# Performance work log

Hardware: AMD Instinct MI355X
Metric: run time of the kernel (lower is better)

## Reference

```python
import jax, jax.numpy as jnp
import numpy as np

# Jamba mamba mixer dims
H = 4096      # hidden_size
D = 8192      # intermediate_size = mamba_expand * hidden_size
N = 16        # ssm_state_size (mamba_d_state)
K = 4         # conv_kernel_size (mamba_d_conv)
R = 256       # time_step_rank (mamba_dt_rank)
BATCH = 1
L = 2048
EPS = 1e-6


def setup_inputs() -> dict:
    key = jax.random.key(0)
    ks = jax.random.split(key, 10)
    s = 0.02
    return {
        "hidden_states": jax.random.normal(ks[0], (BATCH, L, H), jnp.float32),
        "W_in": jax.random.normal(ks[1], (2 * D, H), jnp.float32) * s,
        "conv_w": jax.random.normal(ks[2], (D, K), jnp.float32) * s,
        "conv_b": jax.random.normal(ks[3], (D,), jnp.float32) * s,
        "Wx": jax.random.normal(ks[4], (R + 2 * N, D), jnp.float32) * s,
        "dt_ln_w": jnp.ones((R,), jnp.float32),
        "b_ln_w": jnp.ones((N,), jnp.float32),
        "c_ln_w": jnp.ones((N,), jnp.float32),
        "Wdt": jax.random.normal(ks[5], (D, R), jnp.float32) * s,
        "dt_bias": jax.random.normal(ks[6], (D,), jnp.float32) * s,
        "A": -jnp.exp(jax.random.normal(ks[7], (D, N), jnp.float32) * 0.5),  # A = -exp(A_log)
        "D_param": jnp.ones((D,), jnp.float32),
        "W_out": jax.random.normal(ks[8], (H, D), jnp.float32) * s,
    }


def _rmsnorm(x, w):
    return x * jax.lax.rsqrt(jnp.mean(x * x, axis=-1, keepdims=True) + EPS) * w


def reference(hidden_states, W_in, conv_w, conv_b, Wx, dt_ln_w, b_ln_w, c_ln_w,
              Wdt, dt_bias, A, D_param, W_out):
    # in_proj -> [B, L, 2D]; split into ssm branch and gate
    proj = hidden_states @ W_in.T
    u, gate = jnp.split(proj, 2, axis=-1)

    # causal depthwise conv1d over sequence dim, then SiLU (causal_conv1d_fn)
    x = jnp.transpose(u, (0, 2, 1))  # [B, D, L]
    x = jax.lax.conv_general_dilated(
        x, conv_w[:, None, :], window_strides=(1,), padding=[(K - 1, 0)],
        dimension_numbers=("NCH", "OIH", "NCH"), feature_group_count=D)
    u = jax.nn.silu(jnp.transpose(x, (0, 2, 1)) + conv_b)  # [B, L, D]

    # x_proj -> dt / B / C with RMSNorms
    ssm_p = u @ Wx.T  # [B, L, R + 2N]
    dt, Bm, Cm = jnp.split(ssm_p, [R, R + N], axis=-1)
    dt = _rmsnorm(dt, dt_ln_w)
    Bm = _rmsnorm(Bm, b_ln_w)
    Cm = _rmsnorm(Cm, c_ln_w)

    # dt_proj (skip_bias_add: bias folded into softplus, delta_softplus=True)
    delta = jax.nn.softplus(dt @ Wdt.T + dt_bias)  # [B, L, D]

    # selective scan: state [B, D, N], recurrence over L
    def step(state, xs):
        d_t, B_t, C_t, u_t = xs  # [B,D], [B,N], [B,N], [B,D]
        dA = jnp.exp(d_t[..., None] * A)                       # [B, D, N]
        state = dA * state + (d_t * u_t)[..., None] * B_t[:, None, :]
        y_t = jnp.einsum("bdn,bn->bd", state, C_t)
        return state, y_t

    init = jnp.zeros((hidden_states.shape[0], D, N), hidden_states.dtype)
    xs = (jnp.swapaxes(delta, 0, 1), jnp.swapaxes(Bm, 0, 1),
          jnp.swapaxes(Cm, 0, 1), jnp.swapaxes(u, 0, 1))
    _, ys = jax.lax.scan(step, init, xs)  # ys: [L, B, D]

    y = jnp.swapaxes(ys, 0, 1) + u * D_param   # skip connection u * D
    y = y * jax.nn.silu(gate)                  # gated output
    return y @ W_out.T                         # out_proj -> [B, L, H]
```

## Files before the change

kernel.cpp:

```cpp
#include <hip/hip_runtime.h>
#include <stdint.h>


#define LSEQ 2048
#define HDIM 4096
#define DDIM 8192
#define NST  16
#define NPAD 384
#define NC   32
#define CLEN 64
#define XZK  16

typedef __bf16 bf16x8 __attribute__((ext_vector_type(8)));
typedef float  f32x4  __attribute__((ext_vector_type(4)));

__device__ __forceinline__ ushort f2b(float f) {
  uint32_t x = __float_as_uint(f);
  x += 0x7FFFu + ((x >> 16) & 1u);
  return (ushort)(x >> 16);
}
__device__ __forceinline__ float b2f(ushort u) {
  return __uint_as_float(((uint32_t)u) << 16);
}
__device__ __forceinline__ float b2f_lo(uint u) {
  return __uint_as_float(u << 16);
}
__device__ __forceinline__ float b2f_hi(uint u) {
  return __uint_as_float(u & 0xFFFF0000u);
}

__device__ __forceinline__ void gload_lds16(const ushort* g, ushort* l) {
  __builtin_amdgcn_global_load_lds(
      (const __attribute__((address_space(1))) void*)g,
      (__attribute__((address_space(3))) void*)l, 16, 0, 0);
}

__global__ __launch_bounds__(256) void cvt_kernel(const float* __restrict__ s,
                                                  ushort* __restrict__ d,
                                                  size_t n8) {
  size_t i = (size_t)blockIdx.x * 256 + threadIdx.x;
  if (i >= n8) return;
  const float4* sp = (const float4*)s;
  float4 a = sp[2 * i], b = sp[2 * i + 1];
  union { ushort us[8]; uint4 v; } u;
  u.us[0] = f2b(a.x); u.us[1] = f2b(a.y); u.us[2] = f2b(a.z); u.us[3] = f2b(a.w);
  u.us[4] = f2b(b.x); u.us[5] = f2b(b.y); u.us[6] = f2b(b.z); u.us[7] = f2b(b.w);
  ((uint4*)d)[i] = u.v;
}

template <int MODE, int OUT>
__global__ __launch_bounds__(512, 2) void gemm8p(
    const ushort* __restrict__ A, const ushort* __restrict__ Bw,
    void* __restrict__ Cv, int M, int N, int ldk, int Kc,
    size_t bOffZ, size_t cOffZ) {
  __shared__ __align__(16) ushort As[2][256 * 64];
  __shared__ __align__(16) ushort Bs[2][256 * 64];
  const int tid  = threadIdx.x;
  const int lane = tid & 63;
  const int w    = tid >> 6;
  const int wr   = w >> 2;
  const int wc   = w & 3;

  int mt, nt, zz;
  size_t boff = 0, coff = 0;
  if (MODE == 0) {
    const int bid2 = blockIdx.y * gridDim.x + blockIdx.x;
    const int k8 = bid2 & 7, j = bid2 >> 3;
    mt = j & 7;
    nt = k8 * (gridDim.x >> 3) + (j >> 3);
    zz = 0;
    boff = (size_t)blockIdx.z * bOffZ;
    coff = (size_t)blockIdx.z * cOffZ;
  } else {
    const int glob = (blockIdx.z * gridDim.y + blockIdx.y) * gridDim.x + blockIdx.x;
    const int k8 = glob & 7, j = glob >> 3;
    mt = j & 7;
    nt = (k8 >> 1) * 4 + (j >> 3);
    zz = k8 & 1;
  }
  const int m0 = mt * 256, n0 = nt * 256;
  const int kbeg = zz * Kc;
  const int NT = Kc >> 6;

  const int srck = (lane & 7) ^ ((lane >> 3) & 7);
  const int astripe = w >> 2, awl = w & 3;
  const int arow_st = astripe * 128 + awl * 8 + (lane >> 3);
  const ushort* Abase = A + (size_t)(m0 + arow_st) * ldk + kbeg + srck * 8;
  const int aldsb = (astripe * 128 + awl * 8) * 64;
  const int brow_st = w * 8 + (lane >> 3);
  const ushort* Bbase = Bw + boff + (size_t)(n0 + brow_st) * ldk + kbeg + srck * 8;
  const int bldsb = (w * 8) * 64;

  const int lrow = lane & 15;
  const int kch  = lane >> 4;
  const int axor = lrow & 7;

  auto stA = [&](int buf, int kt, int q) {
    gload_lds16(Abase + (size_t)q * 32 * ldk + kt * 64,
                &As[buf][aldsb + q * 32 * 64]);
  };
  auto stB = [&](int buf, int kt, int half, int jj) {
    gload_lds16(Bbase + (size_t)(half * 128 + jj * 64) * ldk + kt * 64,
                &Bs[buf][bldsb + (half * 128 + jj * 64) * 64]);
  };
  auto rdA = [&](int buf, int mi, int sl) -> bf16x8 {
    int arow = wr * 128 + mi * 16 + lrow;
    int s4 = sl * 4 + kch;
    return *(const bf16x8*)&As[buf][arow * 64 + ((s4 ^ axor) << 3)];
  };
  auto rdB = [&](int buf, int ni, int sl) -> bf16x8 {
    int brow = wc * 64 + ni * 16 + lrow;
    int s4 = sl * 4 + kch;
    return *(const bf16x8*)&Bs[buf][brow * 64 + ((s4 ^ axor) << 3)];
  };

  f32x4 acc[8][4] = {};
  bf16x8 afr[2][2][2];
  bf16x8 bfr[2][4][2];

#define RDAQ(BUF, Q, AP)                                                      \
  { _Pragma("unroll") for (int m2 = 0; m2 < 2; ++m2)                          \
      _Pragma("unroll") for (int sl = 0; sl < 2; ++sl)                        \
        afr[AP][m2][sl] = rdA(BUF, (Q) * 2 + m2, sl); }
#define RDBALL(BUF, BP)                                                       \
  { _Pragma("unroll") for (int ni = 0; ni < 4; ++ni)                          \
      _Pragma("unroll") for (int sl = 0; sl < 2; ++sl)                        \
        bfr[BP][ni][sl] = rdB(BUF, ni, sl); }
#define MFMA16(MQ, AP, BP)                                                    \
  { asm volatile("s_barrier" ::: "memory");                                   \
    __builtin_amdgcn_s_setprio(1);                                            \
    _Pragma("unroll") for (int sl = 0; sl < 2; ++sl)                          \
      _Pragma("unroll") for (int m2 = 0; m2 < 2; ++m2)                        \
        _Pragma("unroll") for (int ni = 0; ni < 4; ++ni)                      \
          acc[(MQ) * 2 + m2][ni] = __builtin_amdgcn_mfma_f32_16x16x32_bf16(   \
              afr[AP][m2][sl], bfr[BP][ni][sl], acc[(MQ) * 2 + m2][ni],       \
              0, 0, 0);                                                       \
    __builtin_amdgcn_s_setprio(0); }

  stB(0, 0, 0, 0); stB(0, 0, 0, 1); stB(0, 0, 1, 0); stB(0, 0, 1, 1);
  stA(0, 0, 0); stA(0, 0, 1); stA(0, 0, 2); stA(0, 0, 3);
  stB(1, 1, 0, 0); stB(1, 1, 0, 1); stB(1, 1, 1, 0); stB(1, 1, 1, 1);
  stA(1, 1, 0); stA(1, 1, 1); stA(1, 1, 2); stA(1, 1, 3);
  asm volatile("s_waitcnt vmcnt(8)" ::: "memory");
  asm volatile("s_barrier" ::: "memory");
  RDBALL(0, 0);
  RDAQ(0, 0, 1);

  for (int t = 0; t < NT; t += 2) {
    const int t2 = (t + 2 < NT) ? t + 2 : 0;
    const int t3 = (t + 3 < NT) ? t + 3 : 0;
    RDAQ(0, 1, 0);
    stB(0, t2, 0, 0); stB(0, t2, 0, 1);
    MFMA16(0, 1, 0);
    RDAQ(0, 2, 1);
    stB(0, t2, 1, 0); stB(0, t2, 1, 1);
    MFMA16(1, 0, 0);
    RDAQ(0, 3, 0);
    stA(0, t2, 0); stA(0, t2, 1);
    MFMA16(2, 1, 0);
    asm volatile("s_waitcnt vmcnt(6)" ::: "memory");
    RDBALL(1, 1);
    RDAQ(1, 0, 1);
    stA(0, t2, 2); stA(0, t2, 3);
    MFMA16(3, 0, 0);
    RDAQ(1, 1, 0);
    stB(1, t3, 0, 0); stB(1, t3, 0, 1);
    MFMA16(0, 1, 1);
    RDAQ(1, 2, 1);
    stB(1, t3, 1, 0); stB(1, t3, 1, 1);
    MFMA16(1, 0, 1);
    RDAQ(1, 3, 0);
    stA(1, t3, 0); stA(1, t3, 1);
    MFMA16(2, 1, 1);
    asm volatile("s_waitcnt vmcnt(6)" ::: "memory");
    RDBALL(0, 0);
    RDAQ(0, 0, 1);
    stA(1, t3, 2); stA(1, t3, 3);
    MFMA16(3, 0, 1);
  }
#undef RDAQ
#undef RDBALL
#undef MFMA16

  asm volatile("s_waitcnt vmcnt(0)" ::: "memory");
  float*  C  = (float*) Cv + (size_t)zz * M * N + coff;
  ushort* Cb = (ushort*)Cv + (size_t)zz * M * N + coff;
#pragma unroll
  for (int mi = 0; mi < 8; ++mi) {
    int row0 = m0 + wr * 128 + mi * 16 + kch * 4;
#pragma unroll
    for (int ni = 0; ni < 4; ++ni) {
      int col = n0 + wc * 64 + ni * 16 + lrow;
#pragma unroll
      for (int q_ = 0; q_ < 4; ++q_) {
        if (OUT == 0)
          C[(size_t)(row0 + q_) * N + col] = acc[mi][ni][q_];
        else
          Cb[(size_t)(row0 + q_) * N + col] = f2b(acc[mi][ni][q_]);
      }
    }
  }
}

template <int EPI, int OBF>
__global__ __launch_bounds__(256) void gemm_nt(
    const ushort* __restrict__ A, const ushort* __restrict__ Bw,
    void* __restrict__ Cv, int M, int N, int ldk, int Kc,
    const float* __restrict__ bias) {
  __shared__ __align__(16) ushort As[128 * 64];
  __shared__ __align__(16) ushort Bs[128 * 64];
  const int tid  = threadIdx.x;
  const int lane = tid & 63;
  const int wid  = tid >> 6;
  const int wr = wid >> 1, wc = wid & 1;
  const int m0 = blockIdx.y * 128, n0 = blockIdx.x * 128;
  const int kbeg = blockIdx.z * Kc;
  float*  C  = (float*) Cv + (size_t)blockIdx.z * M * N;
  ushort* Cb = (ushort*)Cv + (size_t)blockIdx.z * M * N;
  const int rr0 = tid >> 3;
  const int sl  = tid & 7;
  const int lrow = lane & 15;
  const int lks  = lane >> 4;

  f32x4 acc[4][4] = {};

  for (int k0 = kbeg; k0 < kbeg + Kc; k0 += 64) {
#pragma unroll
    for (int i = 0; i < 4; ++i) {
      int rr  = i * 32 + rr0;
      int ksl = sl ^ (rr & 7);
      const ushort* ga = A  + (size_t)(m0 + rr) * ldk + k0 + ksl * 8;
      const ushort* gb = Bw + (size_t)(n0 + rr) * ldk + k0 + ksl * 8;
      ushort* la = As + (i * 256 + (wid << 6)) * 8;
      ushort* lb = Bs + (i * 256 + (wid << 6)) * 8;
      gload_lds16(ga, la);
      gload_lds16(gb, lb);
    }
    __syncthreads();
#pragma unroll
    for (int kc = 0; kc < 2; ++kc) {
      bf16x8 av[4], bv[4];
#pragma unroll
      for (int mi = 0; mi < 4; ++mi) {
        int row = wr * 64 + mi * 16 + lrow;
        int ks  = kc * 4 + lks;
        av[mi] = *(const bf16x8*)(As + row * 64 + ((ks ^ (row & 7)) << 3));
      }
#pragma unroll
      for (int ni = 0; ni < 4; ++ni) {
        int row = wc * 64 + ni * 16 + lrow;
        int ks  = kc * 4 + lks;
        bv[ni] = *(const bf16x8*)(Bs + row * 64 + ((ks ^ (row & 7)) << 3));
      }
#pragma unroll
      for (int mi = 0; mi < 4; ++mi)
#pragma unroll
        for (int ni = 0; ni < 4; ++ni)
          acc[mi][ni] = __builtin_amdgcn_mfma_f32_16x16x32_bf16(
              av[mi], bv[ni], acc[mi][ni], 0, 0, 0);
    }
    __syncthreads();
  }

#pragma unroll
  for (int mi = 0; mi < 4; ++mi) {
    int row0 = m0 + wr * 64 + mi * 16 + (lks << 2);
#pragma unroll
    for (int ni = 0; ni < 4; ++ni) {
      int col = n0 + wc * 64 + ni * 16 + lrow;
      float bcol = 0.f;
      if (EPI == 1) bcol = bias[col];
#pragma unroll
      for (int q = 0; q < 4; ++q) {
        float v = acc[mi][ni][q];
        if (EPI == 1) {
          v += bcol;
          v = (v > 20.f) ? v : log1pf(__expf(v));
        }
        if (OBF == 0) C [(size_t)(row0 + q) * N + col] = v;
        else          Cb[(size_t)(row0 + q) * N + col] = f2b(v);
      }
    }
  }
}

__global__ __launch_bounds__(256) void reduce2_kernel(
    const float* __restrict__ Cp, float* __restrict__ out) {
  size_t i = (size_t)blockIdx.x * 256 + threadIdx.x;
  const size_t MN4 = (size_t)LSEQ * HDIM / 4;
  float4 a = ((const float4*)Cp)[i];
  float4 b = ((const float4*)Cp)[MN4 + i];
  ((float4*)out)[i] = make_float4(a.x + b.x, a.y + b.y, a.z + b.z, a.w + b.w);
}

__global__ __launch_bounds__(256) void conv_silu_kernel(
    const ushort* __restrict__ ub, const float* __restrict__ cw,
    const float* __restrict__ cb, ushort* __restrict__ uc) {
  int d = blockIdx.x * 256 + threadIdx.x;
  int l0 = blockIdx.y * 16;
  float4 w4 = ((const float4*)cw)[d];
  float bsum = cb[d];
  float xm3 = (l0 >= 3) ? b2f(ub[(size_t)(l0 - 3) * DDIM + d]) : 0.f;
  float xm2 = (l0 >= 2) ? b2f(ub[(size_t)(l0 - 2) * DDIM + d]) : 0.f;
  float xm1 = (l0 >= 1) ? b2f(ub[(size_t)(l0 - 1) * DDIM + d]) : 0.f;
#pragma unroll
  for (int i = 0; i < 16; ++i) {
    int l = l0 + i;
    float xc = b2f(ub[(size_t)l * DDIM + d]);
    float s = bsum + w4.x * xm3 + w4.y * xm2 + w4.z * xm1 + w4.w * xc;
    float o = s / (1.f + __expf(-s));
    uc[(size_t)l * DDIM + d] = f2b(o);
    xm3 = xm2; xm2 = xm1; xm1 = xc;
  }
}

__global__ __launch_bounds__(64) void norms_kernel(
    const float* __restrict__ Cp, const float* __restrict__ dtw,
    const float* __restrict__ bw, const float* __restrict__ cwn,
    ushort* __restrict__ dtn, float* __restrict__ Bn, float* __restrict__ Cn) {
  int l = blockIdx.x, lane = threadIdx.x;
  const size_t MN = (size_t)LSEQ * NPAD;
  const float* row = Cp + (size_t)l * NPAD;
  float va[4] = {0.f, 0.f, 0.f, 0.f};
#pragma unroll
  for (int z = 0; z < XZK; ++z) {
    float4 v = ((const float4*)(row + z * MN))[lane];
    va[0] += v.x; va[1] += v.y; va[2] += v.z; va[3] += v.w;
  }
  float ss = va[0]*va[0] + va[1]*va[1] + va[2]*va[2] + va[3]*va[3];
#pragma unroll
  for (int m = 32; m >= 1; m >>= 1) ss += __shfl_xor(ss, m);
  float rs = rsqrtf(ss * (1.f / 256.f) + 1e-6f);
  float4 wv = ((const float4*)dtw)[lane];
  float wa[4] = {wv.x, wv.y, wv.z, wv.w};
  union { ushort us[4]; uint2 v2; } o;
#pragma unroll
  for (int jj = 0; jj < 4; ++jj) o.us[jj] = f2b(va[jj] * rs * wa[jj]);
  ((uint2*)(dtn + (size_t)l * 256))[lane] = o.v2;

  int g = lane & 15;
  float bv = 0.f, cv = 0.f;
#pragma unroll
  for (int z = 0; z < XZK; ++z) {
    bv += row[z * MN + 256 + g];
    cv += row[z * MN + 272 + g];
  }
  float bs = bv * bv, cs = cv * cv;
#pragma unroll
  for (int m = 8; m >= 1; m >>= 1) {
    bs += __shfl_xor(bs, m);
    cs += __shfl_xor(cs, m);
  }
  if (lane < 16) {
    Bn[(size_t)l * NST + lane] = bv * rsqrtf(bs * (1.f / 16.f) + 1e-6f) * bw[lane];
    Cn[(size_t)l * NST + lane] = cv * rsqrtf(cs * (1.f / 16.f) + 1e-6f) * cwn[lane];
  }
}

__global__ __launch_bounds__(256) void scan_phase1(
    const ushort* __restrict__ delta, const ushort* __restrict__ uc,
    const float* __restrict__ Bn, const float* __restrict__ Am,
    float* __restrict__ Sbuf, float* __restrict__ Pbuf) {
  __shared__ float sB[CLEN * NST];
  const int tid = threadIdx.x;
  const int d0 = (blockIdx.x * 256 + tid) * 2;
  const int c = blockIdx.y, l0 = c * CLEN;
  {
    const float4* bsrc = (const float4*)(Bn + (size_t)l0 * NST);
    float4* bdst = (float4*)sB;
    for (int i = tid; i < CLEN * NST / 4; i += 256) bdst[i] = bsrc[i];
  }
  __syncthreads();
  float A[32];
#pragma unroll
  for (int jj = 0; jj < 8; ++jj) {
    float4 a4 = ((const float4*)(Am + (size_t)d0 * NST))[jj];
    A[4*jj] = a4.x; A[4*jj+1] = a4.y; A[4*jj+2] = a4.z; A[4*jj+3] = a4.w;
  }
  float st[32] = {};
  float sda = 0.f, sdb = 0.f;
  const size_t base = ((size_t)l0 * DDIM + d0) >> 1;
  const uint* d32 = (const uint*)delta;
  const uint* u32 = (const uint*)uc;
  const size_t LD2 = DDIM / 2;
  uint dx0 = d32[base], dx1 = d32[base + LD2];
  uint ux0 = u32[base], ux1 = u32[base + LD2];
  for (int l = 0; l < CLEN; l += 2) {
    int lp = (l + 2 < CLEN) ? l + 2 : CLEN - 2;
    uint dxn0 = d32[base + (size_t)lp * LD2];
    uint dxn1 = d32[base + (size_t)(lp + 1) * LD2];
    uint uxn0 = u32[base + (size_t)lp * LD2];
    uint uxn1 = u32[base + (size_t)(lp + 1) * LD2];
    {
      float da = b2f_lo(dx0), db = b2f_hi(dx0);
      float ua = b2f_lo(ux0), ub = b2f_hi(ux0);
      sda += da; sdb += db;
      float dua = da * ua, dub = db * ub;
#pragma unroll
      for (int n = 0; n < 16; ++n) {
        float bn = sB[l * NST + n];
        st[n]      = fmaf(__expf(da * A[n]),      st[n],      dua * bn);
        st[16 + n] = fmaf(__expf(db * A[16 + n]), st[16 + n], dub * bn);
      }
    }
    {
      float da = b2f_lo(dx1), db = b2f_hi(dx1);
      float ua = b2f_lo(ux1), ub = b2f_hi(ux1);
      sda += da; sdb += db;
      float dua = da * ua, dub = db * ub;
#pragma unroll
      for (int n = 0; n < 16; ++n) {
        float bn = sB[(l + 1) * NST + n];
        st[n]      = fmaf(__expf(da * A[n]),      st[n],      dua * bn);
        st[16 + n] = fmaf(__expf(db * A[16 + n]), st[16 + n], dub * bn);
      }
    }
    dx0 = dxn0; dx1 = dxn1; ux0 = uxn0; ux1 = uxn1;
  }
  float4* Sd = (float4*)(Sbuf + ((size_t)c * DDIM + d0) * NST);
  float4* Pd = (float4*)(Pbuf + ((size_t)c * DDIM + d0) * NST);
#pragma unroll
  for (int jj = 0; jj < 8; ++jj) {
    float sd = (jj < 4) ? sda : sdb;
    Sd[jj] = make_float4(st[4*jj], st[4*jj+1], st[4*jj+2], st[4*jj+3]);
    Pd[jj] = make_float4(__expf(A[4*jj] * sd),   __expf(A[4*jj+1] * sd),
                         __expf(A[4*jj+2] * sd), __expf(A[4*jj+3] * sd));
  }
}

__global__ __launch_bounds__(256) void scan_phase2(
    const float* __restrict__ Sbuf, float* __restrict__ Pbuf) {
  size_t t = (size_t)blockIdx.x * 256 + threadIdx.x;
  const size_t stride = (size_t)DDIM * NST;
  float s = 0.f;
  for (int c = 0; c < NC; ++c) {
    float P = Pbuf[c * stride + t];
    float S = Sbuf[c * stride + t];
    Pbuf[c * stride + t] = s;
    s = fmaf(P, s, S);
  }
}

__global__ __launch_bounds__(256) void scan_phase3(
    const ushort* __restrict__ delta, const ushort* __restrict__ uc,
    const float* __restrict__ Bn, const float* __restrict__ Cn,
    const float* __restrict__ Am, const float* __restrict__ Ibuf,
    const ushort* __restrict__ gb, const float* __restrict__ Dp,
    ushort* __restrict__ yg) {
  __shared__ float sB[CLEN * NST];
  __shared__ float sC[CLEN * NST];
  const int tid = threadIdx.x;
  const int d0 = (blockIdx.x * 256 + tid) * 2;
  const int c = blockIdx.y, l0 = c * CLEN;
  {
    const float4* bsrc = (const float4*)(Bn + (size_t)l0 * NST);
    const float4* csrc = (const float4*)(Cn + (size_t)l0 * NST);
    float4* bdst = (float4*)sB;
    float4* cdst = (float4*)sC;
    for (int i = tid; i < CLEN * NST / 4; i += 256) {
      bdst[i] = bsrc[i];
      cdst[i] = csrc[i];
    }
  }
  __syncthreads();
  float A[32], st[32];
#pragma unroll
  for (int jj = 0; jj < 8; ++jj) {
    float4 a4 = ((const float4*)(Am + (size_t)d0 * NST))[jj];
    A[4*jj] = a4.x; A[4*jj+1] = a4.y; A[4*jj+2] = a4.z; A[4*jj+3] = a4.w;
    float4 s4 = ((const float4*)(Ibuf + ((size_t)c * DDIM + d0) * NST))[jj];
    st[4*jj] = s4.x; st[4*jj+1] = s4.y; st[4*jj+2] = s4.z; st[4*jj+3] = s4.w;
  }
  const float2 Dp2 = ((const float2*)Dp)[d0 >> 1];
  const size_t base = ((size_t)l0 * DDIM + d0) >> 1;
  const uint* d32 = (const uint*)delta;
  const uint* u32 = (const uint*)uc;
  const uint* g32 = (const uint*)gb;
  uint* y32 = (uint*)yg;
  const size_t LD2 = DDIM / 2;
  uint dx0 = d32[base], dx1 = d32[base + LD2];
  uint ux0 = u32[base], ux1 = u32[base + LD2];
  uint g0  = g32[base], g1  = g32[base + LD2];
  for (int l = 0; l < CLEN; l += 2) {
    int lp = (l + 2 < CLEN) ? l + 2 : CLEN - 2;
    uint dxn0 = d32[base + (size_t)lp * LD2];
    uint dxn1 = d32[base + (size_t)(lp + 1) * LD2];
    uint uxn0 = u32[base + (size_t)lp * LD2];
    uint uxn1 = u32[base + (size_t)(lp + 1) * LD2];
    uint gn0  = g32[base + (size_t)lp * LD2];
    uint gn1  = g32[base + (size_t)(lp + 1) * LD2];
    {
      float da = b2f_lo(dx0), db = b2f_hi(dx0);
      float ua = b2f_lo(ux0), ub = b2f_hi(ux0);
      float ga = b2f_lo(g0),  gbv = b2f_hi(g0);
      float dua = da * ua, dub = db * ub;
      float ya = 0.f, yb = 0.f;
#pragma unroll
      for (int n = 0; n < 16; ++n) {
        float bn = sB[l * NST + n], cn = sC[l * NST + n];
        st[n]      = fmaf(__expf(da * A[n]),      st[n],      dua * bn);
        st[16 + n] = fmaf(__expf(db * A[16 + n]), st[16 + n], dub * bn);
        ya = fmaf(st[n], cn, ya);
        yb = fmaf(st[16 + n], cn, yb);
      }
      float oa = (ya + ua * Dp2.x) * (ga / (1.f + __expf(-ga)));
      float ob = (yb + ub * Dp2.y) * (gbv / (1.f + __expf(-gbv)));
      y32[base + (size_t)l * LD2] = (uint)f2b(oa) | ((uint)f2b(ob) << 16);
    }
    {
      float da = b2f_lo(dx1), db = b2f_hi(dx1);
      float ua = b2f_lo(ux1), ub = b2f_hi(ux1);
      float ga = b2f_lo(g1),  gbv = b2f_hi(g1);
      float dua = da * ua, dub = db * ub;
      float ya = 0.f, yb = 0.f;
#pragma unroll
      for (int n = 0; n < 16; ++n) {
        float bn = sB[(l + 1) * NST + n], cn = sC[(l + 1) * NST + n];
        st[n]      = fmaf(__expf(da * A[n]),      st[n],      dua * bn);
        st[16 + n] = fmaf(__expf(db * A[16 + n]), st[16 + n], dub * bn);
        ya = fmaf(st[n], cn, ya);
        yb = fmaf(st[16 + n], cn, yb);
      }
      float oa = (ya + ua * Dp2.x) * (ga / (1.f + __expf(-ga)));
      float ob = (yb + ub * Dp2.y) * (gbv / (1.f + __expf(-gbv)));
      y32[base + (size_t)(l + 1) * LD2] = (uint)f2b(oa) | ((uint)f2b(ob) << 16);
    }
    dx0 = dxn0; dx1 = dxn1; ux0 = uxn0; ux1 = uxn1; g0 = gn0; g1 = gn1;
  }
}

extern "C" void kernel_launch(void* const* d_in, const int* in_sizes, int n_in,
                              void* d_out, int out_size, void* d_ws, size_t ws_size,
                              hipStream_t stream) {
  (void)in_sizes; (void)n_in; (void)out_size; (void)ws_size;
  const float* hs   = (const float*)d_in[0];
  const float* W_in = (const float*)d_in[1];
  const float* cw   = (const float*)d_in[2];
  const float* cb   = (const float*)d_in[3];
  const float* Wx   = (const float*)d_in[4];
  const float* dtw  = (const float*)d_in[5];
  const float* bw   = (const float*)d_in[6];
  const float* cwn  = (const float*)d_in[7];
  const float* Wdt  = (const float*)d_in[8];
  const float* dtb  = (const float*)d_in[9];
  const float* Am   = (const float*)d_in[10];
  const float* Dp   = (const float*)d_in[11];
  const float* Wout = (const float*)d_in[12];
  float* out = (float*)d_out;

  char* ws = (char*)d_ws;
  const size_t MB = 1ull << 20;
  ushort* win_b   = (ushort*)(ws);
  ushort* delta_b = (ushort*)(ws);
  ushort* wout_b  = (ushort*)(ws + 64 * MB);
  ushort* ubuf   = (ushort*)(ws + 128 * MB);
  float*  Cp     = (float*) (ws + 128 * MB);
  float*  Cp2    = (float*) (ws + 128 * MB);
  float*  Sbuf   = (float*) (ws + 176 * MB);
  ushort* gbuf   = (ushort*)(ws + 192 * MB);
  float*  Pbuf   = (float*) (ws + 224 * MB);
  ushort* hs_b   = (ushort*)(ws + 256 * MB);
  ushort* wxp_b  = (ushort*)(ws + 272 * MB);
  ushort* wdt_b  = (ushort*)(ws + 278 * MB);
  ushort* ucv    = (ushort*)(ws + 282 * MB);
  ushort* dtn    = (ushort*)(ws + 317 * MB);
  float*  Bn     = (float*) (ws + 318 * MB);
  float*  Cn     = (float*) (ws + 318 * MB + 131072);
  ushort* yg     = (ushort*)(ws + 319 * MB);

  cvt_kernel<<<67108864 / 2048, 256, 0, stream>>>(W_in, win_b, 67108864 / 8);
  cvt_kernel<<<8388608 / 2048, 256, 0, stream>>>(hs, hs_b, 8388608 / 8);
  cvt_kernel<<<2359296 / 2048, 256, 0, stream>>>(Wx, wxp_b, 2359296 / 8);
  hipMemsetAsync((char*)wxp_b + 4718592, 0, 1572864, stream);
  cvt_kernel<<<2097152 / 2048, 256, 0, stream>>>(Wdt, wdt_b, 2097152 / 8);

  gemm8p<0, 1><<<dim3(32, 8, 2), 512, 0, stream>>>(
      hs_b, win_b, ubuf, 2048, DDIM, 4096, 4096,
      (size_t)DDIM * 4096, (size_t)(gbuf - ubuf));
  cvt_kernel<<<33554432 / 2048, 256, 0, stream>>>(Wout, wout_b, 33554432 / 8);

  conv_silu_kernel<<<dim3(32, 128), 256, 0, stream>>>(ubuf, cw, cb, ucv);

  gemm_nt<0, 0><<<dim3(3, 16, XZK), 256, 0, stream>>>(ucv, wxp_b, Cp,
                                                      2048, NPAD, 8192,
                                                      8192 / XZK, nullptr);
  norms_kernel<<<2048, 64, 0, stream>>>(Cp, dtw, bw, cwn, dtn, Bn, Cn);

  gemm_nt<1, 1><<<dim3(64, 16), 256, 0, stream>>>(dtn, wdt_b, delta_b,
                                                  2048, DDIM, 256, 256, dtb);

  scan_phase1<<<dim3(16, NC), 256, 0, stream>>>(delta_b, ucv, Bn, Am, Sbuf, Pbuf);
  scan_phase2<<<512, 256, 0, stream>>>(Sbuf, Pbuf);
  scan_phase3<<<dim3(16, NC), 256, 0, stream>>>(delta_b, ucv, Bn, Cn, Am, Pbuf,
                                                gbuf, Dp, yg);

  gemm8p<1, 0><<<dim3(16, 8, 2), 512, 0, stream>>>(yg, wout_b, Cp2,
                                                   2048, HDIM, 8192, 4096, 0, 0);
  reduce2_kernel<<<(LSEQ * HDIM / 4) / 256, 256, 0, stream>>>(Cp2, out);
}
```

Baseline: 825.7 us.

## Merge weight conversions into one kernel, halve scan chunks and x_proj split-K

Replaces five separate fp32-to-bf16 conversion launches with one multi-tensor kernel that processes 16 elements per thread, and moves the W_out conversion ahead of the first GEMM. The scan chunk count drops from 32 to 16 with 128-step chunks, and the x_proj split-K factor drops from 16 to 8, which shrinks the partial-sum traffic in the norms kernel. Explicit lgkmcnt waits are added before barriers in the bf16 GEMM, which may add stalls in exchange for correct LDS ordering. Buffers are relocated in the workspace so the early W_out copy does not overlap other buffers.

```diff
diff --git a/kernel.cpp b/kernel.cpp
--- a/kernel.cpp
+++ b/kernel.cpp
@@ -7,9 +7,8 @@
 #define DDIM 8192
 #define NST  16
 #define NPAD 384
-#define NC   32
-#define CLEN 64
-#define XZK  16
+#define NC   16
+#define CLEN 128
 
 typedef __bf16 bf16x8 __attribute__((ext_vector_type(8)));
 typedef float  f32x4  __attribute__((ext_vector_type(4)));
@@ -35,17 +34,30 @@
       (__attribute__((address_space(3))) void*)l, 16, 0, 0);
 }
 
-__global__ __launch_bounds__(256) void cvt_kernel(const float* __restrict__ s,
-                                                  ushort* __restrict__ d,
-                                                  size_t n8) {
-  size_t i = (size_t)blockIdx.x * 256 + threadIdx.x;
-  if (i >= n8) return;
-  const float4* sp = (const float4*)s;
-  float4 a = sp[2 * i], b = sp[2 * i + 1];
-  union { ushort us[8]; uint4 v; } u;
-  u.us[0] = f2b(a.x); u.us[1] = f2b(a.y); u.us[2] = f2b(a.z); u.us[3] = f2b(a.w);
-  u.us[4] = f2b(b.x); u.us[5] = f2b(b.y); u.us[6] = f2b(b.z); u.us[7] = f2b(b.w);
-  ((uint4*)d)[i] = u.v;
+__global__ __launch_bounds__(256) void cvt5_kernel(
+    const float* __restrict__ s0, ushort* __restrict__ d0,
+    const float* __restrict__ s1, ushort* __restrict__ d1,
+    const float* __restrict__ s2, ushort* __restrict__ d2,
+    const float* __restrict__ s3, ushort* __restrict__ d3,
+    const float* __restrict__ s4, ushort* __restrict__ d4,
+    int o1, int o2, int o3, int o4) {
+  int b = blockIdx.x;
+  const float* s; ushort* d; int lb;
+  if (b < o1)      { s = s0; d = d0; lb = b; }
+  else if (b < o2) { s = s1; d = d1; lb = b - o1; }
+  else if (b < o3) { s = s2; d = d2; lb = b - o2; }
+  else if (b < o4) { s = s3; d = d3; lb = b - o3; }
+  else             { s = s4; d = d4; lb = b - o4; }
+  size_t i = (size_t)lb * 256 + threadIdx.x;
+  const float4* sp = (const float4*)s + i * 4;
+  float4 a0 = sp[0], a1 = sp[1], a2 = sp[2], a3 = sp[3];
+  union { ushort us[8]; uint4 v; } u0, u1;
+  u0.us[0] = f2b(a0.x); u0.us[1] = f2b(a0.y); u0.us[2] = f2b(a0.z); u0.us[3] = f2b(a0.w);
+  u0.us[4] = f2b(a1.x); u0.us[5] = f2b(a1.y); u0.us[6] = f2b(a1.z); u0.us[7] = f2b(a1.w);
+  u1.us[0] = f2b(a2.x); u1.us[1] = f2b(a2.y); u1.us[2] = f2b(a2.z); u1.us[3] = f2b(a2.w);
+  u1.us[4] = f2b(a3.x); u1.us[5] = f2b(a3.y); u1.us[6] = f2b(a3.z); u1.us[7] = f2b(a3.w);
+  ((uint4*)d)[i * 2]     = u0.v;
+  ((uint4*)d)[i * 2 + 1] = u1.v;
 }
 
 template <int MODE, int OUT>
@@ -127,7 +139,8 @@
       _Pragma("unroll") for (int sl = 0; sl < 2; ++sl)                        \
         bfr[BP][ni][sl] = rdB(BUF, ni, sl); }
 #define MFMA16(MQ, AP, BP)                                                    \
-  { asm volatile("s_barrier" ::: "memory");                                   \
+  { asm volatile("s_waitcnt lgkmcnt(0)" ::: "memory");                        \
+    asm volatile("s_barrier" ::: "memory");                                   \
     __builtin_amdgcn_s_setprio(1);                                            \
     _Pragma("unroll") for (int sl = 0; sl < 2; ++sl)                          \
       _Pragma("unroll") for (int m2 = 0; m2 < 2; ++m2)                        \
@@ -145,6 +158,8 @@
   asm volatile("s_barrier" ::: "memory");
   RDBALL(0, 0);
   RDAQ(0, 0, 1);
+  asm volatile("s_waitcnt lgkmcnt(0)" ::: "memory");
+  asm volatile("s_barrier" ::: "memory");
 
   for (int t = 0; t < NT; t += 2) {
     const int t2 = (t + 2 < NT) ? t + 2 : 0;
@@ -323,7 +338,7 @@
   const float* row = Cp + (size_t)l * NPAD;
   float va[4] = {0.f, 0.f, 0.f, 0.f};
 #pragma unroll
-  for (int z = 0; z < XZK; ++z) {
+  for (int z = 0; z < 8; ++z) {
     float4 v = ((const float4*)(row + z * MN))[lane];
     va[0] += v.x; va[1] += v.y; va[2] += v.z; va[3] += v.w;
   }
@@ -341,7 +356,7 @@
   int g = lane & 15;
   float bv = 0.f, cv = 0.f;
 #pragma unroll
-  for (int z = 0; z < XZK; ++z) {
+  for (int z = 0; z < 8; ++z) {
     bv += row[z * MN + 256 + g];
     cv += row[z * MN + 272 + g];
   }
@@ -552,13 +567,12 @@
   const size_t MB = 1ull << 20;
   ushort* win_b   = (ushort*)(ws);
   ushort* delta_b = (ushort*)(ws);
-  ushort* wout_b  = (ushort*)(ws + 64 * MB);
   ushort* ubuf   = (ushort*)(ws + 128 * MB);
   float*  Cp     = (float*) (ws + 128 * MB);
   float*  Cp2    = (float*) (ws + 128 * MB);
-  float*  Sbuf   = (float*) (ws + 176 * MB);
+  float*  Sbuf   = (float*) (ws + 152 * MB);
+  float*  Pbuf   = (float*) (ws + 160 * MB);
   ushort* gbuf   = (ushort*)(ws + 192 * MB);
-  float*  Pbuf   = (float*) (ws + 224 * MB);
   ushort* hs_b   = (ushort*)(ws + 256 * MB);
   ushort* wxp_b  = (ushort*)(ws + 272 * MB);
   ushort* wdt_b  = (ushort*)(ws + 278 * MB);
@@ -567,23 +581,22 @@
   float*  Bn     = (float*) (ws + 318 * MB);
   float*  Cn     = (float*) (ws + 318 * MB + 131072);
   ushort* yg     = (ushort*)(ws + 319 * MB);
-
-  cvt_kernel<<<67108864 / 2048, 256, 0, stream>>>(W_in, win_b, 67108864 / 8);
-  cvt_kernel<<<8388608 / 2048, 256, 0, stream>>>(hs, hs_b, 8388608 / 8);
-  cvt_kernel<<<2359296 / 2048, 256, 0, stream>>>(Wx, wxp_b, 2359296 / 8);
+  ushort* wout_b = (ushort*)(ws + 352 * MB);
+
+  cvt5_kernel<<<27712, 256, 0, stream>>>(
+      W_in, win_b, hs, hs_b, Wx, wxp_b, Wdt, wdt_b, Wout, wout_b,
+      16384, 18432, 19008, 19520);
   hipMemsetAsync((char*)wxp_b + 4718592, 0, 1572864, stream);
-  cvt_kernel<<<2097152 / 2048, 256, 0, stream>>>(Wdt, wdt_b, 2097152 / 8);
 
   gemm8p<0, 1><<<dim3(32, 8, 2), 512, 0, stream>>>(
       hs_b, win_b, ubuf, 2048, DDIM, 4096, 4096,
       (size_t)DDIM * 4096, (size_t)(gbuf - ubuf));
-  cvt_kernel<<<33554432 / 2048, 256, 0, stream>>>(Wout, wout_b, 33554432 / 8);
 
   conv_silu_kernel<<<dim3(32, 128), 256, 0, stream>>>(ubuf, cw, cb, ucv);
 
-  gemm_nt<0, 0><<<dim3(3, 16, XZK), 256, 0, stream>>>(ucv, wxp_b, Cp,
-                                                      2048, NPAD, 8192,
-                                                      8192 / XZK, nullptr);
+  gemm_nt<0, 0><<<dim3(3, 16, 8), 256, 0, stream>>>(ucv, wxp_b, Cp,
+                                                    2048, NPAD, 8192, 1024,
+                                                    nullptr);
   norms_kernel<<<2048, 64, 0, stream>>>(Cp, dtw, bw, cwn, dtn, Bn, Cn);
 
   gemm_nt<1, 1><<<dim3(64, 16), 256, 0, stream>>>(dtn, wdt_b, delta_b,
```

After: 818.6 us (median of 2 runs). About the same (-0.9%).
